# Optimization experiments

Measured on AMD Instinct MI355X. Metric: run time of the kernel, lower is better.

Reference implementation:

```python
import jax, jax.numpy as jnp
import numpy as np

D_MODEL = 1024
N_HEADS = 16
HEAD_DIM = D_MODEL // N_HEADS


def setup_inputs() -> dict:
    key = jax.random.key(0)
    k1, k2, k3 = jax.random.split(key, 3)
    scale = 0.02
    x = jax.random.normal(k1, (2, 2048, D_MODEL), dtype=jnp.float32)
    w_qkv = jax.random.normal(k2, (D_MODEL, 3 * D_MODEL), dtype=jnp.float32) * scale
    b_qkv = jnp.zeros((3 * D_MODEL,), dtype=jnp.float32)
    w_proj = jax.random.normal(k3, (D_MODEL, D_MODEL), dtype=jnp.float32) * scale
    b_proj = jnp.zeros((D_MODEL,), dtype=jnp.float32)
    return {"x": x, "w_qkv": w_qkv, "b_qkv": b_qkv, "w_proj": w_proj, "b_proj": b_proj}


def reference(x, w_qkv, b_qkv, w_proj, b_proj):
    bsz, seq_len, d_model = x.shape
    qkv = x @ w_qkv + b_qkv  # [B,S,3D]
    q, k, v = jnp.split(qkv, 3, axis=-1)
    # [B,S,D] -> [B,H,S,hd]
    def to_heads(t):
        return t.reshape(bsz, seq_len, N_HEADS, HEAD_DIM).transpose(0, 2, 1, 3)
    q, k, v = to_heads(q), to_heads(k), to_heads(v)
    scores = jnp.einsum("bhqd,bhkd->bhqk", q, k) / jnp.sqrt(jnp.float32(HEAD_DIM))
    causal = jnp.triu(jnp.ones((seq_len, seq_len), dtype=bool), k=1)
    scores = jnp.where(causal, -jnp.inf, scores)
    attn = jax.nn.softmax(scores, axis=-1)
    out = jnp.einsum("bhqk,bhkd->bhqd", attn, v)  # [B,H,S,hd]
    out = out.transpose(0, 2, 1, 3).reshape(bsz, seq_len, d_model)
    return out @ w_proj + b_proj
```

## Files before the change

kernel.cpp:

```cpp
#include <hip/hip_runtime.h>
#include <hip/hip_bf16.h>

#define D_MODEL 1024
#define SEQ     2048
#define NH      16
#define HD      64
#define M_TOK   4096
#define THREE_D 3072

using bf16x8 = __bf16 __attribute__((ext_vector_type(8)));
using bf16x4 = __bf16 __attribute__((ext_vector_type(4)));
using f32x4  = float  __attribute__((ext_vector_type(4)));

typedef __attribute__((address_space(3))) uint32_t lds_u32;
typedef const __attribute__((address_space(1))) uint32_t glb_u32;

__global__ __launch_bounds__(256) void cast_kernel(const float* __restrict__ in,
                                                   __bf16* __restrict__ out, int n4) {
  int i = blockIdx.x * 256 + threadIdx.x;
  if (i < n4) {
    float4 f = reinterpret_cast<const float4*>(in)[i];
    bf16x4 o;
    o[0] = (__bf16)f.x; o[1] = (__bf16)f.y; o[2] = (__bf16)f.z; o[3] = (__bf16)f.w;
    reinterpret_cast<bf16x4*>(out)[i] = o;
  }
}

__global__ __launch_bounds__(256) void transpose_cast(const float* __restrict__ in,
                                                      __bf16* __restrict__ out, int R, int C) {
  __shared__ float tile[64][65];
  int c0 = blockIdx.x * 64, r0 = blockIdx.y * 64;
  int tx = threadIdx.x & 63, ty = threadIdx.x >> 6;
#pragma unroll
  for (int i = 0; i < 16; ++i) {
    int r = ty + i * 4;
    tile[r][tx] = in[(size_t)(r0 + r) * C + c0 + tx];
  }
  __syncthreads();
#pragma unroll
  for (int i = 0; i < 16; ++i) {
    int r = ty + i * 4;
    out[(size_t)(c0 + r) * R + r0 + tx] = (__bf16)tile[tx][r];
  }
}

__global__ __launch_bounds__(256, 3) void gemm_qkv(const __bf16* __restrict__ A,
                                                   const __bf16* __restrict__ BT,
                                                   const float* __restrict__ bias,
                                                   __bf16* __restrict__ qb, __bf16* __restrict__ kb,
                                                   __bf16* __restrict__ vb) {
  __shared__ __bf16 As[2][128 * 32];
  __shared__ __bf16 Bs[2][128 * 32];
  const int Kdim = D_MODEL;
  const int tid  = threadIdx.x;
  const int lane = tid & 63, wave = tid >> 6;
  const int lr = lane & 15, lg = lane >> 4;
  const int wm = (wave >> 1) * 64, wn = (wave & 1) * 64;

  const int f   = blockIdx.x;
  const int swz = (f & 7) * 96 + (f >> 3);
  const int m0  = (swz / 24) * 128, n0 = (swz % 24) * 128;

  const int srow = tid >> 2, scol = (tid & 3) * 8;

  f32x4 acc[4][4] = {};

  const __bf16* aSrc = A  + (size_t)(m0 + srow) * Kdim + scol;
  const __bf16* bSrc = BT + (size_t)(n0 + srow) * Kdim + scol;

  auto stage = [&](int p, int k0) {
    __builtin_amdgcn_global_load_lds((glb_u32*)(aSrc + k0),              (lds_u32*)(As[p] + wave * 512),        16, 0, 0);
    __builtin_amdgcn_global_load_lds((glb_u32*)(aSrc + 64 * Kdim + k0), (lds_u32*)(As[p] + wave * 512 + 2048), 16, 0, 0);
    __builtin_amdgcn_global_load_lds((glb_u32*)(bSrc + k0),              (lds_u32*)(Bs[p] + wave * 512),        16, 0, 0);
    __builtin_amdgcn_global_load_lds((glb_u32*)(bSrc + 64 * Kdim + k0), (lds_u32*)(Bs[p] + wave * 512 + 2048), 16, 0, 0);
  };

  stage(0, 0);
  const int nk = Kdim / 32;
  for (int kk = 0; kk < nk; ++kk) {
    const int cur = kk & 1;
    if (kk + 1 < nk) {
      stage(cur ^ 1, (kk + 1) * 32);
      asm volatile("s_waitcnt vmcnt(4)" ::: "memory");
    } else {
      asm volatile("s_waitcnt vmcnt(0)" ::: "memory");
    }
    __syncthreads();

    bf16x8 af[4], bfv[4];
#pragma unroll
    for (int i = 0; i < 4; ++i) af[i]  = *reinterpret_cast<const bf16x8*>(&As[cur][(wm + i * 16 + lr) * 32 + lg * 8]);
#pragma unroll
    for (int j = 0; j < 4; ++j) bfv[j] = *reinterpret_cast<const bf16x8*>(&Bs[cur][(wn + j * 16 + lr) * 32 + lg * 8]);
#pragma unroll
    for (int i = 0; i < 4; ++i)
#pragma unroll
      for (int j = 0; j < 4; ++j)
        acc[i][j] = __builtin_amdgcn_mfma_f32_16x16x32_bf16(af[i], bfv[j], acc[i][j], 0, 0, 0);

    __syncthreads();
  }

#pragma unroll
  for (int i = 0; i < 4; ++i) {
#pragma unroll
    for (int j = 0; j < 4; ++j) {
      const int gc = n0 + wn + j * 16 + lr;
      const float bv = bias[gc];
      const int t = gc >> 10, rem = gc & 1023;
      const int h = rem >> 6, d = rem & 63;
#pragma unroll
      for (int ii = 0; ii < 4; ++ii) {
        const int gr = m0 + wm + i * 16 + lg * 4 + ii;
        const float val = acc[i][j][ii] + bv;
        const int b = gr >> 11, s = gr & 2047;
        if (t == 0) {
          qb[(((size_t)(b * NH + h)) * SEQ + s) * HD + d] = (__bf16)(val * 0.125f);
        } else if (t == 1) {
          kb[(((size_t)(b * NH + h)) * SEQ + s) * HD + d] = (__bf16)val;
        } else {
          vb[(((size_t)(b * NH + h)) * HD + d) * SEQ + s] = (__bf16)val;
        }
      }
    }
  }
}

__global__ __launch_bounds__(256, 4) void gemm_proj(const __bf16* __restrict__ A,
                                                    const __bf16* __restrict__ BT,
                                                    const float* __restrict__ bias,
                                                    float* __restrict__ fout) {
  __shared__ __bf16 As[2][64 * 32];
  __shared__ __bf16 Bs[2][128 * 32];
  const int Kdim = D_MODEL;
  const int tid  = threadIdx.x;
  const int lane = tid & 63, wave = tid >> 6;
  const int lr = lane & 15, lg = lane >> 4;
  const int wm = (wave >> 1) * 32, wn = (wave & 1) * 64;

  const int f   = blockIdx.x;
  const int swz = (f & 7) * 64 + (f >> 3);
  const int n0  = (swz & 7) * 128, m0 = (swz >> 3) * 64;

  const int srow = tid >> 2, scol = (tid & 3) * 8;

  f32x4 acc[2][4] = {};

  const __bf16* aSrc = A  + (size_t)(m0 + srow) * Kdim + scol;
  const __bf16* bSrc = BT + (size_t)(n0 + srow) * Kdim + scol;

  auto stage = [&](int p, int k0) {
    if (wave == 0 || wave == 1)
      ;
    __builtin_amdgcn_global_load_lds((glb_u32*)(aSrc + k0),              (lds_u32*)(As[p] + wave * 512),        16, 0, 0);
    __builtin_amdgcn_global_load_lds((glb_u32*)(bSrc + k0),              (lds_u32*)(Bs[p] + wave * 512),        16, 0, 0);
    __builtin_amdgcn_global_load_lds((glb_u32*)(bSrc + 64 * Kdim + k0), (lds_u32*)(Bs[p] + wave * 512 + 2048), 16, 0, 0);
  };

  stage(0, 0);
  const int nk = Kdim / 32;
  for (int kk = 0; kk < nk; ++kk) {
    const int cur = kk & 1;
    if (kk + 1 < nk) {
      stage(cur ^ 1, (kk + 1) * 32);
      asm volatile("s_waitcnt vmcnt(3)" ::: "memory");
    } else {
      asm volatile("s_waitcnt vmcnt(0)" ::: "memory");
    }
    __syncthreads();

    bf16x8 af[2], bfv[4];
#pragma unroll
    for (int i = 0; i < 2; ++i) af[i]  = *reinterpret_cast<const bf16x8*>(&As[cur][(wm + i * 16 + lr) * 32 + lg * 8]);
#pragma unroll
    for (int j = 0; j < 4; ++j) bfv[j] = *reinterpret_cast<const bf16x8*>(&Bs[cur][(wn + j * 16 + lr) * 32 + lg * 8]);
#pragma unroll
    for (int i = 0; i < 2; ++i)
#pragma unroll
      for (int j = 0; j < 4; ++j)
        acc[i][j] = __builtin_amdgcn_mfma_f32_16x16x32_bf16(af[i], bfv[j], acc[i][j], 0, 0, 0);

    __syncthreads();
  }

#pragma unroll
  for (int i = 0; i < 2; ++i) {
#pragma unroll
    for (int j = 0; j < 4; ++j) {
      const int gc = n0 + wn + j * 16 + lr;
      const float bv = bias[gc];
#pragma unroll
      for (int ii = 0; ii < 4; ++ii) {
        const int gr = m0 + wm + i * 16 + lg * 4 + ii;
        fout[(size_t)gr * D_MODEL + gc] = acc[i][j][ii] + bv;
      }
    }
  }
}

__global__ __launch_bounds__(256, 4) void attn_kernel(const __bf16* __restrict__ Q,
                                                      const __bf16* __restrict__ K,
                                                      const __bf16* __restrict__ VT,
                                                      __bf16* __restrict__ AO) {
  __shared__ __bf16 Kb[2][64 * 64];
  __shared__ __bf16 Vb[2][64 * 64];
  __shared__ __bf16 Ps[4][16 * 64];

  const int tid  = threadIdx.x;
  const int lane = tid & 63, wave = tid >> 6;
  const int lr = lane & 15, lg = lane >> 4;

  const int f  = blockIdx.x;
  const int c  = f & 7;
  const int u  = f >> 3;
  const int bh = c * 4 + (u & 3);
  const int s2 = u >> 2, grp = s2 >> 3, r = s2 & 7;
  const int qblk = (grp == 0) ? (31 - r) : (grp == 1) ? r : (grp == 2) ? (39 - s2) : (s2 - 16);

  const int q0 = qblk * 64 + wave * 16;
  const size_t base = (size_t)bh * SEQ * HD;
  const char* Kg  = (const char*)(K + base);
  const char* VTg = (const char*)(VT + base);

  bf16x8 qf[2];
#pragma unroll
  for (int kc = 0; kc < 2; ++kc)
    qf[kc] = *reinterpret_cast<const bf16x8*>(Q + base + (size_t)(q0 + lr) * HD + kc * 32 + lg * 8);

  float lrun[4] = {0.f, 0.f, 0.f, 0.f};
  f32x4 o[4] = {};

  const int nt = qblk + 1;
  const int nmaxF = (wave | 1) + 1;

  auto stage = [&](int bufp, int t) {
    const int k0 = t * 64;
#pragma unroll
    for (int p = 0; p < 2; ++p) {
      const int row = wave * 16 + p * 8 + (lane >> 3);
      {
        const int srcOff = (k0 + row) * 128 + (((lane & 7) ^ (row & 7)) << 4);
        __builtin_amdgcn_global_load_lds((glb_u32*)(Kg + srcOff),
                                         (lds_u32*)&Kb[bufp][(wave * 16 + p * 8) * 64], 16, 0, 0);
      }
      {
        const int srcOff = row * 4096 + k0 * 2 + (((lane & 7) ^ (row & 7)) << 4);
        __builtin_amdgcn_global_load_lds((glb_u32*)(VTg + srcOff),
                                         (lds_u32*)&Vb[bufp][(wave * 16 + p * 8) * 64], 16, 0, 0);
      }
    }
  };

  stage(0, 0);
  asm volatile("s_waitcnt vmcnt(0)" ::: "memory");
  __syncthreads();

  for (int t = 0; t < nt; ++t) {
    const int p = t & 1;
    const int k0 = t * 64;
    const bool last = (t == nt - 1);
    const int nmax = last ? nmaxF : 4;
    const int kcmax = nmax >> 1;

    if (t + 1 < nt) stage(p ^ 1, t + 1);

    const __bf16* Kt = Kb[p];
    const __bf16* Vt = Vb[p];

    f32x4 s[4] = {};
#pragma unroll
    for (int kc = 0; kc < 2; ++kc) {
#pragma unroll
      for (int n = 0; n < 4; ++n)
        if (n < nmax) {
          bf16x8 kf = *reinterpret_cast<const bf16x8*>(
              &Kt[(n * 16 + lr) * 64 + (((kc * 4 + lg) ^ (lr & 7)) << 3)]);
          s[n] = __builtin_amdgcn_mfma_f32_16x16x32_bf16(qf[kc], kf, s[n], 0, 0, 0);
        }
    }

    if (last) {
#pragma unroll
      for (int n = 0; n < 4; ++n)
        if (n < nmax)
#pragma unroll
          for (int ii = 0; ii < 4; ++ii) {
            int qg = q0 + lg * 4 + ii;
            int kg = k0 + n * 16 + lr;
            if (kg > qg) s[n][ii] = -__builtin_inff();
          }
    }

#pragma unroll
    for (int n = 0; n < 4; ++n)
      if (n < nmax)
#pragma unroll
        for (int ii = 0; ii < 4; ++ii) {
          float pv = __expf(s[n][ii]);
          lrun[ii] += pv;
          const int row = lg * 4 + ii;
          Ps[wave][row * 64 + (((n * 2 + (lr >> 3)) ^ (row & 7)) << 3) + (lr & 7)] = (__bf16)pv;
        }

#pragma unroll
    for (int kc = 0; kc < 2; ++kc)
      if (kc < kcmax) {
        bf16x8 pa = *reinterpret_cast<const bf16x8*>(
            &Ps[wave][lr * 64 + (((kc * 4 + lg) ^ (lr & 7)) << 3)]);
#pragma unroll
        for (int nd = 0; nd < 4; ++nd) {
          bf16x8 vf = *reinterpret_cast<const bf16x8*>(
              &Vt[(nd * 16 + lr) * 64 + (((kc * 4 + lg) ^ (lr & 7)) << 3)]);
          o[nd] = __builtin_amdgcn_mfma_f32_16x16x32_bf16(pa, vf, o[nd], 0, 0, 0);
        }
      }

    asm volatile("s_waitcnt vmcnt(0)" ::: "memory");
    __syncthreads();
  }

#pragma unroll
  for (int off = 1; off <= 8; off <<= 1)
#pragma unroll
    for (int ii = 0; ii < 4; ++ii) lrun[ii] += __shfl_xor(lrun[ii], off, 64);

  const int b = bh >> 4, h = bh & 15;
  float rl[4];
#pragma unroll
  for (int ii = 0; ii < 4; ++ii) rl[ii] = 1.f / lrun[ii];
#pragma unroll
  for (int nd = 0; nd < 4; ++nd)
#pragma unroll
    for (int ii = 0; ii < 4; ++ii) {
      int row = q0 + lg * 4 + ii;
      AO[((size_t)(b * SEQ) + row) * D_MODEL + h * HD + nd * 16 + lr] = (__bf16)(o[nd][ii] * rl[ii]);
    }
}

extern "C" void kernel_launch(void* const* d_in, const int* in_sizes, int n_in,
                              void* d_out, int out_size, void* d_ws, size_t ws_size,
                              hipStream_t stream) {
  const float* x      = (const float*)d_in[0];
  const float* w_qkv  = (const float*)d_in[1];
  const float* b_qkv  = (const float*)d_in[2];
  const float* w_proj = (const float*)d_in[3];
  const float* b_proj = (const float*)d_in[4];
  float* out = (float*)d_out;

  char* ws = (char*)d_ws;
  __bf16* xb     = (__bf16*)(ws);
  __bf16* wqkvT  = (__bf16*)(ws + 8388608);
  __bf16* wprojT = (__bf16*)(ws + 14680064);
  __bf16* qb     = (__bf16*)(ws + 16777216);
  __bf16* kb     = (__bf16*)(ws + 25165824);
  __bf16* vtb    = (__bf16*)(ws + 33554432);
  __bf16* ao     = (__bf16*)(ws + 41943040);

  cast_kernel<<<4096, 256, 0, stream>>>(x, xb, M_TOK * D_MODEL / 4);
  transpose_cast<<<dim3(THREE_D / 64, D_MODEL / 64), 256, 0, stream>>>(w_qkv, wqkvT, D_MODEL, THREE_D);
  transpose_cast<<<dim3(D_MODEL / 64, D_MODEL / 64), 256, 0, stream>>>(w_proj, wprojT, D_MODEL, D_MODEL);

  gemm_qkv<<<768, 256, 0, stream>>>(xb, wqkvT, b_qkv, qb, kb, vtb);

  attn_kernel<<<1024, 256, 0, stream>>>(qb, kb, vtb, ao);

  gemm_proj<<<512, 256, 0, stream>>>(ao, wprojT, b_proj, out);
}
```

Before: 115.4 us.

## Rewrite QKV GEMM with 256x256 tiles, 8 waves, swizzled LDS and phased MFMA

The QKV projection GEMM moves from 128x128 tiles with 4 waves to 256x256 tiles with 8 waves and a K step of 64. LDS columns are XOR-swizzled to avoid bank conflicts. Each iteration splits its MFMA work into four sub-phases, with barriers and s_setprio so compute overlaps LDS reads and the next global-to-LDS prefetch. This cuts global and LDS traffic per FLOP but leaves only 192 blocks at one block per CU, which may underfill the 256 CUs.

```diff
diff --git a/kernel.cpp b/kernel.cpp
--- a/kernel.cpp
+++ b/kernel.cpp
@@ -44,75 +44,151 @@
   }
 }
 
-__global__ __launch_bounds__(256, 3) void gemm_qkv(const __bf16* __restrict__ A,
+__global__ __launch_bounds__(512, 1) void gemm_qkv(const __bf16* __restrict__ A,
                                                    const __bf16* __restrict__ BT,
                                                    const float* __restrict__ bias,
                                                    __bf16* __restrict__ qb, __bf16* __restrict__ kb,
                                                    __bf16* __restrict__ vb) {
-  __shared__ __bf16 As[2][128 * 32];
-  __shared__ __bf16 Bs[2][128 * 32];
-  const int Kdim = D_MODEL;
+  __shared__ __bf16 Al[2][256 * 64];
+  __shared__ __bf16 Bl[2][256 * 64];
+
   const int tid  = threadIdx.x;
   const int lane = tid & 63, wave = tid >> 6;
   const int lr = lane & 15, lg = lane >> 4;
-  const int wm = (wave >> 1) * 64, wn = (wave & 1) * 64;
+  const int wm = wave >> 2, wn = wave & 3;
+  const int xorc = lr & 7;
 
   const int f   = blockIdx.x;
-  const int swz = (f & 7) * 96 + (f >> 3);
-  const int m0  = (swz / 24) * 128, n0 = (swz % 24) * 128;
-
-  const int srow = tid >> 2, scol = (tid & 3) * 8;
-
-  f32x4 acc[4][4] = {};
-
-  const __bf16* aSrc = A  + (size_t)(m0 + srow) * Kdim + scol;
-  const __bf16* bSrc = BT + (size_t)(n0 + srow) * Kdim + scol;
-
-  auto stage = [&](int p, int k0) {
-    __builtin_amdgcn_global_load_lds((glb_u32*)(aSrc + k0),              (lds_u32*)(As[p] + wave * 512),        16, 0, 0);
-    __builtin_amdgcn_global_load_lds((glb_u32*)(aSrc + 64 * Kdim + k0), (lds_u32*)(As[p] + wave * 512 + 2048), 16, 0, 0);
-    __builtin_amdgcn_global_load_lds((glb_u32*)(bSrc + k0),              (lds_u32*)(Bs[p] + wave * 512),        16, 0, 0);
-    __builtin_amdgcn_global_load_lds((glb_u32*)(bSrc + 64 * Kdim + k0), (lds_u32*)(Bs[p] + wave * 512 + 2048), 16, 0, 0);
+  const int swz = (f & 7) * 24 + (f >> 3);
+  const int m0  = (swz / 12) * 256, n0 = (swz % 12) * 256;
+
+  const int sRow = lane >> 3;
+  const int sCol = ((lane & 7) ^ sRow) * 8;
+
+  f32x4 acc[8][4] = {};
+
+  auto stageTile = [&](int ps, int kt) {
+#pragma unroll
+    for (int L = 0; L < 4; ++L) {
+      const int r = (wave * 4 + (L & 3)) * 8;
+      __builtin_amdgcn_global_load_lds(
+          (glb_u32*)(A + (size_t)(m0 + r + sRow) * 1024 + kt * 64 + sCol),
+          (lds_u32*)(&Al[ps][0] + r * 64), 16, 0, 0);
+    }
+#pragma unroll
+    for (int L = 0; L < 4; ++L) {
+      const int r = (wave * 4 + (L & 3)) * 8;
+      __builtin_amdgcn_global_load_lds(
+          (glb_u32*)(BT + (size_t)(n0 + r + sRow) * 1024 + kt * 64 + sCol),
+          (lds_u32*)(&Bl[ps][0] + r * 64), 16, 0, 0);
+    }
   };
 
-  stage(0, 0);
-  const int nk = Kdim / 32;
-  for (int kk = 0; kk < nk; ++kk) {
-    const int cur = kk & 1;
-    if (kk + 1 < nk) {
-      stage(cur ^ 1, (kk + 1) * 32);
-      asm volatile("s_waitcnt vmcnt(4)" ::: "memory");
-    } else {
-      asm volatile("s_waitcnt vmcnt(0)" ::: "memory");
-    }
-    __syncthreads();
-
-    bf16x8 af[4], bfv[4];
-#pragma unroll
-    for (int i = 0; i < 4; ++i) af[i]  = *reinterpret_cast<const bf16x8*>(&As[cur][(wm + i * 16 + lr) * 32 + lg * 8]);
-#pragma unroll
-    for (int j = 0; j < 4; ++j) bfv[j] = *reinterpret_cast<const bf16x8*>(&Bs[cur][(wn + j * 16 + lr) * 32 + lg * 8]);
-#pragma unroll
-    for (int i = 0; i < 4; ++i)
-#pragma unroll
-      for (int j = 0; j < 4; ++j)
-        acc[i][j] = __builtin_amdgcn_mfma_f32_16x16x32_bf16(af[i], bfv[j], acc[i][j], 0, 0, 0);
-
-    __syncthreads();
-  }
-
-#pragma unroll
-  for (int i = 0; i < 4; ++i) {
-#pragma unroll
-    for (int j = 0; j < 4; ++j) {
-      const int gc = n0 + wn + j * 16 + lr;
+
+  stageTile(0, 0);
+  asm volatile("s_waitcnt vmcnt(0)" ::: "memory");
+  __builtin_amdgcn_s_barrier();
+
+  const int NK = 16;
+  for (int kt = 0; kt < NK; ++kt) {
+    const int cur = kt & 1;
+    if (kt + 1 < NK) stageTile(cur ^ 1, kt + 1);
+
+    const __bf16* At = &Al[cur][0];
+    const __bf16* Bt = &Bl[cur][0];
+    bf16x8 a[4][2], b0[2][2], b1[2][2];
+
+#pragma unroll
+    for (int fm = 0; fm < 4; ++fm)
+#pragma unroll
+      for (int kk = 0; kk < 2; ++kk)
+        a[fm][kk] = *reinterpret_cast<const bf16x8*>(
+            &At[(wm * 128 + fm * 16 + lr) * 64 + (((kk * 4 + lg) ^ xorc) << 3)]);
+#pragma unroll
+    for (int fn = 0; fn < 2; ++fn)
+#pragma unroll
+      for (int kk = 0; kk < 2; ++kk)
+        b0[fn][kk] = *reinterpret_cast<const bf16x8*>(
+            &Bt[(wn * 64 + fn * 16 + lr) * 64 + (((kk * 4 + lg) ^ xorc) << 3)]);
+    __builtin_amdgcn_s_barrier();
+    asm volatile("s_waitcnt lgkmcnt(0)" ::: "memory");
+    __builtin_amdgcn_sched_barrier(0);
+    __builtin_amdgcn_s_setprio(1);
+#pragma unroll
+    for (int kk = 0; kk < 2; ++kk)
+#pragma unroll
+      for (int fm = 0; fm < 4; ++fm)
+#pragma unroll
+        for (int fn = 0; fn < 2; ++fn)
+          acc[fm][fn] = __builtin_amdgcn_mfma_f32_16x16x32_bf16(a[fm][kk], b0[fn][kk], acc[fm][fn], 0, 0, 0);
+    __builtin_amdgcn_s_setprio(0);
+    __builtin_amdgcn_s_barrier();
+
+#pragma unroll
+    for (int fn = 0; fn < 2; ++fn)
+#pragma unroll
+      for (int kk = 0; kk < 2; ++kk)
+        b1[fn][kk] = *reinterpret_cast<const bf16x8*>(
+            &Bt[(wn * 64 + (2 + fn) * 16 + lr) * 64 + (((kk * 4 + lg) ^ xorc) << 3)]);
+    __builtin_amdgcn_s_barrier();
+    asm volatile("s_waitcnt lgkmcnt(0)" ::: "memory");
+    __builtin_amdgcn_sched_barrier(0);
+    __builtin_amdgcn_s_setprio(1);
+#pragma unroll
+    for (int kk = 0; kk < 2; ++kk)
+#pragma unroll
+      for (int fm = 0; fm < 4; ++fm)
+#pragma unroll
+        for (int fn = 0; fn < 2; ++fn)
+          acc[fm][2 + fn] = __builtin_amdgcn_mfma_f32_16x16x32_bf16(a[fm][kk], b1[fn][kk], acc[fm][2 + fn], 0, 0, 0);
+    __builtin_amdgcn_s_setprio(0);
+    __builtin_amdgcn_s_barrier();
+
+#pragma unroll
+    for (int fm = 0; fm < 4; ++fm)
+#pragma unroll
+      for (int kk = 0; kk < 2; ++kk)
+        a[fm][kk] = *reinterpret_cast<const bf16x8*>(
+            &At[(wm * 128 + 64 + fm * 16 + lr) * 64 + (((kk * 4 + lg) ^ xorc) << 3)]);
+    __builtin_amdgcn_s_barrier();
+    asm volatile("s_waitcnt lgkmcnt(0)" ::: "memory");
+    __builtin_amdgcn_sched_barrier(0);
+    __builtin_amdgcn_s_setprio(1);
+#pragma unroll
+    for (int kk = 0; kk < 2; ++kk)
+#pragma unroll
+      for (int fm = 0; fm < 4; ++fm)
+#pragma unroll
+        for (int fn = 0; fn < 2; ++fn)
+          acc[4 + fm][fn] = __builtin_amdgcn_mfma_f32_16x16x32_bf16(a[fm][kk], b0[fn][kk], acc[4 + fm][fn], 0, 0, 0);
+    __builtin_amdgcn_s_setprio(0);
+    __builtin_amdgcn_s_barrier();
+
+    __builtin_amdgcn_s_setprio(1);
+#pragma unroll
+    for (int kk = 0; kk < 2; ++kk)
+#pragma unroll
+      for (int fm = 0; fm < 4; ++fm)
+#pragma unroll
+        for (int fn = 0; fn < 2; ++fn)
+          acc[4 + fm][2 + fn] = __builtin_amdgcn_mfma_f32_16x16x32_bf16(a[fm][kk], b1[fn][kk], acc[4 + fm][2 + fn], 0, 0, 0);
+    __builtin_amdgcn_s_setprio(0);
+    asm volatile("s_waitcnt vmcnt(0)" ::: "memory");
+    __builtin_amdgcn_s_barrier();
+  }
+
+#pragma unroll
+  for (int fm = 0; fm < 8; ++fm) {
+#pragma unroll
+    for (int fn = 0; fn < 4; ++fn) {
+      const int gc = n0 + wn * 64 + fn * 16 + lr;
       const float bv = bias[gc];
       const int t = gc >> 10, rem = gc & 1023;
       const int h = rem >> 6, d = rem & 63;
 #pragma unroll
       for (int ii = 0; ii < 4; ++ii) {
-        const int gr = m0 + wm + i * 16 + lg * 4 + ii;
-        const float val = acc[i][j][ii] + bv;
+        const int gr = m0 + wm * 128 + fm * 16 + lg * 4 + ii;
+        const float val = acc[fm][fn][ii] + bv;
         const int b = gr >> 11, s = gr & 2047;
         if (t == 0) {
           qb[(((size_t)(b * NH + h)) * SEQ + s) * HD + d] = (__bf16)(val * 0.125f);
@@ -150,8 +226,6 @@
   const __bf16* bSrc = BT + (size_t)(n0 + srow) * Kdim + scol;
 
   auto stage = [&](int p, int k0) {
-    if (wave == 0 || wave == 1)
-      ;
     __builtin_amdgcn_global_load_lds((glb_u32*)(aSrc + k0),              (lds_u32*)(As[p] + wave * 512),        16, 0, 0);
     __builtin_amdgcn_global_load_lds((glb_u32*)(bSrc + k0),              (lds_u32*)(Bs[p] + wave * 512),        16, 0, 0);
     __builtin_amdgcn_global_load_lds((glb_u32*)(bSrc + 64 * Kdim + k0), (lds_u32*)(Bs[p] + wave * 512 + 2048), 16, 0, 0);
@@ -360,7 +434,7 @@
   transpose_cast<<<dim3(THREE_D / 64, D_MODEL / 64), 256, 0, stream>>>(w_qkv, wqkvT, D_MODEL, THREE_D);
   transpose_cast<<<dim3(D_MODEL / 64, D_MODEL / 64), 256, 0, stream>>>(w_proj, wprojT, D_MODEL, D_MODEL);
 
-  gemm_qkv<<<768, 256, 0, stream>>>(xb, wqkvT, b_qkv, qb, kb, vtb);
+  gemm_qkv<<<192, 512, 0, stream>>>(xb, wqkvT, b_qkv, qb, kb, vtb);
 
   attn_kernel<<<1024, 256, 0, stream>>>(qb, kb, vtb, ao);
 
```

Measured after the change: 138.3 us. 1.2x slower.

## Triple-buffer GEMM LDS staging, use raw barriers, drop block swizzle

Applied to the files above, without the earlier changes.

Both GEMMs move from double to triple buffering of LDS tiles, issuing loads two K-steps ahead with matching vmcnt waits. __syncthreads is replaced by explicit s_barrier, with an lgkmcnt wait before the trailing barrier. The XCD/L2-aware block-index swizzle is replaced by a plain 2D grid. The goal is to hide more global-load latency. The cost is more LDS per block, which may reduce occupancy in gemm_qkv (48KB per block), and losing the swizzle may hurt cache locality.

```diff
diff --git a/kernel.cpp b/kernel.cpp
--- a/kernel.cpp
+++ b/kernel.cpp
@@ -49,18 +49,14 @@
                                                    const float* __restrict__ bias,
                                                    __bf16* __restrict__ qb, __bf16* __restrict__ kb,
                                                    __bf16* __restrict__ vb) {
-  __shared__ __bf16 As[2][128 * 32];
-  __shared__ __bf16 Bs[2][128 * 32];
+  __shared__ __bf16 As[3][128 * 32];
+  __shared__ __bf16 Bs[3][128 * 32];
   const int Kdim = D_MODEL;
   const int tid  = threadIdx.x;
   const int lane = tid & 63, wave = tid >> 6;
   const int lr = lane & 15, lg = lane >> 4;
   const int wm = (wave >> 1) * 64, wn = (wave & 1) * 64;
-
-  const int f   = blockIdx.x;
-  const int swz = (f & 7) * 96 + (f >> 3);
-  const int m0  = (swz / 24) * 128, n0 = (swz % 24) * 128;
-
+  const int m0 = blockIdx.y * 128, n0 = blockIdx.x * 128;
   const int srow = tid >> 2, scol = (tid & 3) * 8;
 
   f32x4 acc[4][4] = {};
@@ -75,17 +71,20 @@
     __builtin_amdgcn_global_load_lds((glb_u32*)(bSrc + 64 * Kdim + k0), (lds_u32*)(Bs[p] + wave * 512 + 2048), 16, 0, 0);
   };
 
+  const int nk = Kdim / 32;
   stage(0, 0);
-  const int nk = Kdim / 32;
+  stage(1, 32);
   for (int kk = 0; kk < nk; ++kk) {
-    const int cur = kk & 1;
-    if (kk + 1 < nk) {
-      stage(cur ^ 1, (kk + 1) * 32);
+    const int cur = kk % 3;
+    if (kk + 2 < nk) {
+      stage((kk + 2) % 3, (kk + 2) * 32);
+      asm volatile("s_waitcnt vmcnt(8)" ::: "memory");
+    } else if (kk + 1 < nk) {
       asm volatile("s_waitcnt vmcnt(4)" ::: "memory");
     } else {
       asm volatile("s_waitcnt vmcnt(0)" ::: "memory");
     }
-    __syncthreads();
+    __builtin_amdgcn_s_barrier();
 
     bf16x8 af[4], bfv[4];
 #pragma unroll
@@ -98,7 +97,8 @@
       for (int j = 0; j < 4; ++j)
         acc[i][j] = __builtin_amdgcn_mfma_f32_16x16x32_bf16(af[i], bfv[j], acc[i][j], 0, 0, 0);
 
-    __syncthreads();
+    asm volatile("s_waitcnt lgkmcnt(0)" ::: "memory");
+    __builtin_amdgcn_s_barrier();
   }
 
 #pragma unroll
@@ -130,18 +130,14 @@
                                                     const __bf16* __restrict__ BT,
                                                     const float* __restrict__ bias,
                                                     float* __restrict__ fout) {
-  __shared__ __bf16 As[2][64 * 32];
-  __shared__ __bf16 Bs[2][128 * 32];
+  __shared__ __bf16 As[3][64 * 32];
+  __shared__ __bf16 Bs[3][128 * 32];
   const int Kdim = D_MODEL;
   const int tid  = threadIdx.x;
   const int lane = tid & 63, wave = tid >> 6;
   const int lr = lane & 15, lg = lane >> 4;
   const int wm = (wave >> 1) * 32, wn = (wave & 1) * 64;
-
-  const int f   = blockIdx.x;
-  const int swz = (f & 7) * 64 + (f >> 3);
-  const int n0  = (swz & 7) * 128, m0 = (swz >> 3) * 64;
-
+  const int n0 = blockIdx.x * 128, m0 = blockIdx.y * 64;
   const int srow = tid >> 2, scol = (tid & 3) * 8;
 
   f32x4 acc[2][4] = {};
@@ -150,24 +146,25 @@
   const __bf16* bSrc = BT + (size_t)(n0 + srow) * Kdim + scol;
 
   auto stage = [&](int p, int k0) {
-    if (wave == 0 || wave == 1)
-      ;
     __builtin_amdgcn_global_load_lds((glb_u32*)(aSrc + k0),              (lds_u32*)(As[p] + wave * 512),        16, 0, 0);
     __builtin_amdgcn_global_load_lds((glb_u32*)(bSrc + k0),              (lds_u32*)(Bs[p] + wave * 512),        16, 0, 0);
     __builtin_amdgcn_global_load_lds((glb_u32*)(bSrc + 64 * Kdim + k0), (lds_u32*)(Bs[p] + wave * 512 + 2048), 16, 0, 0);
   };
 
+  const int nk = Kdim / 32;
   stage(0, 0);
-  const int nk = Kdim / 32;
+  stage(1, 32);
   for (int kk = 0; kk < nk; ++kk) {
-    const int cur = kk & 1;
-    if (kk + 1 < nk) {
-      stage(cur ^ 1, (kk + 1) * 32);
+    const int cur = kk % 3;
+    if (kk + 2 < nk) {
+      stage((kk + 2) % 3, (kk + 2) * 32);
+      asm volatile("s_waitcnt vmcnt(6)" ::: "memory");
+    } else if (kk + 1 < nk) {
       asm volatile("s_waitcnt vmcnt(3)" ::: "memory");
     } else {
       asm volatile("s_waitcnt vmcnt(0)" ::: "memory");
     }
-    __syncthreads();
+    __builtin_amdgcn_s_barrier();
 
     bf16x8 af[2], bfv[4];
 #pragma unroll
@@ -180,7 +177,8 @@
       for (int j = 0; j < 4; ++j)
         acc[i][j] = __builtin_amdgcn_mfma_f32_16x16x32_bf16(af[i], bfv[j], acc[i][j], 0, 0, 0);
 
-    __syncthreads();
+    asm volatile("s_waitcnt lgkmcnt(0)" ::: "memory");
+    __builtin_amdgcn_s_barrier();
   }
 
 #pragma unroll
@@ -360,9 +358,11 @@
   transpose_cast<<<dim3(THREE_D / 64, D_MODEL / 64), 256, 0, stream>>>(w_qkv, wqkvT, D_MODEL, THREE_D);
   transpose_cast<<<dim3(D_MODEL / 64, D_MODEL / 64), 256, 0, stream>>>(w_proj, wprojT, D_MODEL, D_MODEL);
 
-  gemm_qkv<<<768, 256, 0, stream>>>(xb, wqkvT, b_qkv, qb, kb, vtb);
+  gemm_qkv<<<dim3(THREE_D / 128, M_TOK / 128), 256, 0, stream>>>(
+      xb, wqkvT, b_qkv, qb, kb, vtb);
 
   attn_kernel<<<1024, 256, 0, stream>>>(qb, kb, vtb, ao);
 
-  gemm_proj<<<512, 256, 0, stream>>>(ao, wprojT, b_proj, out);
-}
+  gemm_proj<<<dim3(D_MODEL / 128, M_TOK / 64), 256, 0, stream>>>(
+      ao, wprojT, b_proj, out);
+}
```

Result: no change. 114.6 us (-0.7%).
